# Kernel tuning notes

Measured on AMD Instinct MI355X. Metric: run time of the kernel, lower is better.

## Reference

```python
import jax, jax.numpy as jnp
import numpy as np

LN_EPS = 1e-5
NEG_SLOPE = 0.01  # torch F.leaky_relu default


def setup_inputs() -> dict:
    key = jax.random.key(0)
    ks = jax.random.split(key, 12)
    B, N, Do, Na = 128, 32, 128, 16
    H, Dk, Dv = 4, 64, 64
    Dio = Do + Na  # 144
    g = lambda k, shape, fan_in: jax.random.normal(k, shape, jnp.float32) / np.sqrt(fan_in)
    return {
        "states": jax.random.normal(ks[0], (B, N, Do), jnp.float32),
        "policies": jax.random.uniform(ks[1], (B, N, Na), jnp.float32),
        "actions": jax.random.uniform(ks[2], (B, N, Na), jnp.float32),
        "W_se": g(ks[3], (Do, 128), Do),
        "b_se": jnp.zeros((128,), jnp.float32),
        "W_sape": g(ks[4], (Dio, 128), Dio),
        "b_sape": jnp.zeros((128,), jnp.float32),
        "Wk": g(ks[5], (H, 128, Dk), 128),
        "Wq": g(ks[6], (H, 128, Dk), 128),
        "Wv": g(ks[7], (H, 128, Dv), 128),
        "ln_g": jnp.ones((H, Dv), jnp.float32),
        "ln_b": jnp.zeros((H, Dv), jnp.float32),
        "W_f1": g(ks[8], (H * Dv, 64), H * Dv),
        "W_f2": g(ks[9], (64, 1), 64),
    }


def _layernorm(x, g, b):
    mu = x.mean(-1, keepdims=True)
    var = ((x - mu) ** 2).mean(-1, keepdims=True)
    return (x - mu) * jax.lax.rsqrt(var + LN_EPS) * g + b


def reference(states, policies, actions, W_se, b_se, W_sape, b_sape,
              Wk, Wq, Wv, ln_g, ln_b, W_f1, W_f2):
    leaky = lambda x: jax.nn.leaky_relu(x, NEG_SLOPE)
    B, N, _ = states.shape
    H, _, Dv = Wv.shape
    d_k = Wk.shape[-1]

    se = leaky(states @ W_se + b_se)  # [B,N,128]

    oa = jnp.concatenate([states, actions], axis=-1)   # [B,N,Dio]
    op = jnp.concatenate([states, policies], axis=-1)  # [B,N,Dio]
    # oap[b,j,k] = op[b,k] if j==k else oa[b,k]  (place_policies/place_actions masks)
    eye = jnp.eye(N, dtype=states.dtype)[None, :, :, None]  # [1,N,N,1]
    oap = eye * op[:, None, :, :] + (1.0 - eye) * oa[:, None, :, :]  # [B,N,N,Dio]
    x = leaky(oap @ W_sape + b_sape)  # [B,N,N,128]

    key = jnp.einsum('bnd,hde->bhne', se, Wk)  # [B,H,N,Dk]
    qry = jnp.einsum('bnd,hde->bhne', se, Wq)
    scores = jnp.einsum('bhie,bhke->bhik', qry, key) / jnp.sqrt(jnp.asarray(d_k, states.dtype))
    w = jax.nn.softmax(scores, axis=-1)  # [B,H,N,N]

    av = jnp.einsum('bjkd,hde->bhjke', x, Wv)  # [B,H,N,N,Dv]
    # node_features[b,h,i,j] = sum_k w[b,h,i,k] * av[b,h,j,k]  (fuses torch's O(N^3) repeat)
    nf = jnp.einsum('bhik,bhjke->bhije', w, av)  # [B,H,N,N,Dv]
    nf = _layernorm(nf, ln_g[None, :, None, None, :], ln_b[None, :, None, None, :])

    mh = jnp.moveaxis(nf, 1, 3).reshape(B, N, N, H * Dv)  # concat heads on last dim
    value = leaky(mh @ W_f1) @ W_f2  # [B,N,N,1]
    return value, w
```

## Files before the change

### kernel.cpp

```cpp
#include <hip/hip_runtime.h>
#include <hip/hip_bf16.h>

#define B 128
#define N 32
#define DO 128
#define NA 16
#define H 4
#define DK 64
#define DV 64
#define LN_EPS 1e-5f
#define NEG_SLOPE 0.01f

typedef unsigned short u16;
typedef __attribute__((ext_vector_type(8))) short bf16x8;
typedef __attribute__((ext_vector_type(4))) float f32x4;

__device__ __forceinline__ float leaky(float x) {
    return x >= 0.f ? x : NEG_SLOPE * x;
}

__device__ __forceinline__ u16 f2bf(float x) {
    union { float f; unsigned int u; } v; v.f = x;
    unsigned int r = (v.u + 0x7FFF + ((v.u >> 16) & 1)) >> 16;
    return (u16)r;
}

__device__ __forceinline__ float bf2f(u16 x) {
    union { unsigned int u; float f; } v; v.u = ((unsigned int)x) << 16;
    return v.f;
}

__global__ __launch_bounds__(256) void kP(
    const float* __restrict__ Wk, const float* __restrict__ Wq,
    const float* __restrict__ Wv, const float* __restrict__ W_se,
    const float* __restrict__ W_sape, const float* __restrict__ ln_g,
    const float* __restrict__ ln_b, const float* __restrict__ W_f1,
    u16* __restrict__ wTb, u16* __restrict__ wseT, u16* __restrict__ wsapeT,
    u16* __restrict__ sapeTail, u16* __restrict__ wTg,
    float* __restrict__ GW, float* __restrict__ BW)
{
    const int blk = blockIdx.x;
    const int t   = threadIdx.x;
    __shared__ float wls[8192];

    if (blk < 4) {
        const int hh = blk;
        for (int m = 0; m < 3; m++) {
            const float* src = (m == 0 ? Wq : (m == 1 ? Wk : Wv)) + hh * 8192;
            for (int idx = t; idx < 2048; idx += 256)
                ((float4*)wls)[idx] = ((const float4*)src)[idx];
            __syncthreads();
            u16* dst = wTb + (hh * 3 + m) * 8192;
            for (int idx = t; idx < 8192; idx += 256) {
                const int n = idx >> 7, k = idx & 127;
                dst[idx] = f2bf(wls[k * 64 + n]);
            }
            __syncthreads();
        }
    } else if (blk == 4 || blk == 5) {
        const float* src = (blk == 4) ? W_se : W_sape;
        u16* dst = (blk == 4) ? wseT : wsapeT;
        for (int chunk = 0; chunk < 2; chunk++) {
            const int k0 = chunk * 64;
            for (int idx = t; idx < 2048; idx += 256)
                ((float4*)wls)[idx] = ((const float4*)(src + k0 * 128))[idx];
            __syncthreads();
            for (int idx = t; idx < 8192; idx += 256) {
                const int n = idx >> 6, kk = idx & 63;
                dst[n * 128 + k0 + kk] = f2bf(wls[kk * 128 + n]);
            }
            __syncthreads();
        }
        if (blk == 5) {
            for (int idx = t; idx < 2048; idx += 256)
                wls[idx] = W_sape[128 * 128 + idx];
            __syncthreads();
            for (int idx = t; idx < 4096; idx += 256) {
                const int n = idx >> 5, kk = idx & 31;
                sapeTail[n * 32 + kk] = (kk < 16) ? f2bf(wls[kk * 128 + n]) : (u16)0;
            }
        }
    } else {
        for (int idx = t; idx < 16384; idx += 256) {
            const int hh = idx >> 12, c = (idx >> 6) & 63, ee = idx & 63;
            wTg[idx] = f2bf(ln_g[hh * 64 + ee] * W_f1[(hh * 64 + ee) * 64 + c]);
        }
        {
            const int hh = t >> 6, c = t & 63;
            float g = 0.f;
            #pragma unroll 4
            for (int ee = 0; ee < 64; ee++)
                g += ln_g[hh * 64 + ee] * W_f1[(hh * 64 + ee) * 64 + c];
            GW[t] = g;
        }
        {
            const int c = t & 63, qq = t >> 6;
            float bacc = 0.f;
            #pragma unroll 4
            for (int r = 0; r < 64; r++)
                bacc += ln_b[qq * 64 + r] * W_f1[(qq * 64 + r) * 64 + c];
            wls[qq * 64 + c] = bacc;
        }
        __syncthreads();
        if (t < 64) BW[t] = wls[t] + wls[64 + t] + wls[128 + t] + wls[192 + t];
    }
}

__global__ __launch_bounds__(1024, 8) void kB(
    const float* __restrict__ states, const float* __restrict__ actions,
    const float* __restrict__ policies,
    const float* __restrict__ b_se, const float* __restrict__ b_sape,
    const u16* __restrict__ wTb, const u16* __restrict__ wseT,
    const u16* __restrict__ wsapeT, const u16* __restrict__ sapeTail,
    const u16* __restrict__ wTg,
    float* __restrict__ w_out,
    float* __restrict__ SG, float* __restrict__ DG,
    float* __restrict__ sumS, float* __restrict__ sumS2,
    float* __restrict__ sumD, float* __restrict__ sumD2,
    float* __restrict__ dotSD)
{
    const int bh   = blockIdx.x;
    const int b    = bh >> 2;
    const int h    = bh & 3;
    const int t    = threadIdx.x;
    const int wave = t >> 6;
    const int e    = t & 63;
    const int q16  = e >> 4;
    const int l16  = e & 15;

    __shared__ alignas(16) u16   sST[32 * 136];
    __shared__ alignas(16) u16   actA[32 * 40];
    __shared__ alignas(16) u16   polA[32 * 40];
    __shared__ alignas(16) u16   sSE[32 * 136];
    __shared__ alignas(16) u16   sXA[32 * 136];
    __shared__ alignas(16) u16   sXP[32 * 136];
    __shared__ alignas(16) u16   qb[32 * 72];
    __shared__ alignas(16) u16   kb[32 * 72];
    __shared__ alignas(16) u16   avaT[64 * 40];
    __shared__ alignas(16) u16   diffb[32 * 72];
    __shared__ alignas(16) u16   wb[32 * 40];
    __shared__ alignas(16) float S32[32 * 68];
    __shared__ alignas(16) u16   Sb[32 * 72];

    {
        const int r = t >> 5, c4 = (t & 31) * 4;
        const float4 s4 = *(const float4*)&states[(b * 32 + r) * 128 + c4];
        ushort4 u;
        u.x = f2bf(s4.x); u.y = f2bf(s4.y); u.z = f2bf(s4.z); u.w = f2bf(s4.w);
        *(ushort4*)&sST[r * 136 + c4] = u;
    }
    if (t < 512) {
        const int r = t >> 4, c = t & 15;
        actA[r * 40 + c]      = f2bf(actions[(b * 32 + r) * 16 + c]);
        actA[r * 40 + 16 + c] = 0;
    } else {
        const int t2 = t - 512, r = t2 >> 4, c = t2 & 15;
        polA[r * 40 + c]      = f2bf(policies[(b * 32 + r) * 16 + c]);
        polA[r * 40 + 16 + c] = 0;
    }
    __syncthreads();

    {
        const int mt = wave >> 3, nt = wave & 7;
        const int arow = mt * 16 + l16;
        const int bcol = nt * 16 + l16;
        f32x4 a_se = {0.f,0.f,0.f,0.f}, a_sp = {0.f,0.f,0.f,0.f};
        f32x4 a_oa = {0.f,0.f,0.f,0.f}, a_op = {0.f,0.f,0.f,0.f};
        const u16* bse_p = wseT + bcol * 128;
        const u16* bsp_p = wsapeT + bcol * 128;
        #pragma unroll
        for (int ks = 0; ks < 4; ks++) {
            const bf16x8 af = *(const bf16x8*)&sST[arow * 136 + ks * 32 + q16 * 8];
            a_se = __builtin_amdgcn_mfma_f32_16x16x32_bf16(
                af, *(const bf16x8*)&bse_p[ks * 32 + q16 * 8], a_se, 0, 0, 0);
            a_sp = __builtin_amdgcn_mfma_f32_16x16x32_bf16(
                af, *(const bf16x8*)&bsp_p[ks * 32 + q16 * 8], a_sp, 0, 0, 0);
        }
        const bf16x8 bt = *(const bf16x8*)&sapeTail[bcol * 32 + q16 * 8];
        a_oa = __builtin_amdgcn_mfma_f32_16x16x32_bf16(
            *(const bf16x8*)&actA[arow * 40 + q16 * 8], bt, a_oa, 0, 0, 0);
        a_op = __builtin_amdgcn_mfma_f32_16x16x32_bf16(
            *(const bf16x8*)&polA[arow * 40 + q16 * 8], bt, a_op, 0, 0, 0);
        const float bse_c = b_se[bcol];
        const float bsp_c = b_sape[bcol];
        const int r0 = mt * 16 + q16 * 4;
        #pragma unroll
        for (int v = 0; v < 4; v++) {
            sSE[(r0 + v) * 136 + bcol] = f2bf(leaky(a_se[v] + bse_c));
            sXA[(r0 + v) * 136 + bcol] = f2bf(leaky(a_sp[v] + a_oa[v] + bsp_c));
            sXP[(r0 + v) * 136 + bcol] = f2bf(leaky(a_sp[v] + a_op[v] + bsp_c));
        }
    }
    __syncthreads();

    f32x4 acc[2];
    #pragma unroll
    for (int p = 0; p < 2; p++) {
        const int tau = wave * 2 + p;
        const int mat = tau >> 3;
        const int mt  = (tau >> 2) & 1, nt = tau & 3;
        const u16* X  = (mat <= 1) ? sSE : (mat == 2 ? sXA : sXP);
        const int widx = (mat == 0) ? 0 : (mat == 1 ? 1 : 2);
        const int arow = mt * 16 + l16;
        const u16* wsrc = wTb + ((h * 3 + widx) * 64 + nt * 16 + l16) * 128;
        f32x4 a = {0.f, 0.f, 0.f, 0.f};
        #pragma unroll
        for (int ks = 0; ks < 4; ks++) {
            const bf16x8 af = *(const bf16x8*)&X[arow * 136 + ks * 32 + q16 * 8];
            const bf16x8 bf = *(const bf16x8*)&wsrc[ks * 32 + q16 * 8];
            a = __builtin_amdgcn_mfma_f32_16x16x32_bf16(af, bf, a, 0, 0, 0);
        }
        acc[p] = a;
    }
    #pragma unroll
    for (int p = 0; p < 2; p++) {
        const int tau = wave * 2 + p;
        const int mat = tau >> 3;
        const int mt  = (tau >> 2) & 1, nt = tau & 3;
        const int c   = nt * 16 + l16;
        const int r0  = mt * 16 + q16 * 4;
        if (mat == 0) {
            #pragma unroll
            for (int v = 0; v < 4; v++) qb[(r0 + v) * 72 + c] = f2bf(acc[p][v]);
        } else if (mat == 1) {
            #pragma unroll
            for (int v = 0; v < 4; v++) kb[(r0 + v) * 72 + c] = f2bf(acc[p][v]);
        } else if (mat == 2) {
            #pragma unroll
            for (int v = 0; v < 4; v++) avaT[c * 40 + (r0 + v)] = f2bf(acc[p][v]);
        }
    }
    __syncthreads();

    if (wave < 2) {
        const int mt = wave;
        f32x4 s0 = {0.f,0.f,0.f,0.f}, s1 = {0.f,0.f,0.f,0.f};
        #pragma unroll
        for (int ks = 0; ks < 2; ks++) {
            const bf16x8 af = *(const bf16x8*)&qb[(mt * 16 + l16) * 72 + ks * 32 + q16 * 8];
            const bf16x8 b0 = *(const bf16x8*)&kb[l16 * 72 + ks * 32 + q16 * 8];
            const bf16x8 b1 = *(const bf16x8*)&kb[(16 + l16) * 72 + ks * 32 + q16 * 8];
            s0 = __builtin_amdgcn_mfma_f32_16x16x32_bf16(af, b0, s0, 0, 0, 0);
            s1 = __builtin_amdgcn_mfma_f32_16x16x32_bf16(af, b1, s1, 0, 0, 0);
        }
        #pragma unroll
        for (int v = 0; v < 4; v++) {
            float a0 = s0[v] * 0.125f, a1 = s1[v] * 0.125f;
            float mx = fmaxf(a0, a1);
            #pragma unroll
            for (int m = 1; m < 16; m <<= 1) mx = fmaxf(mx, __shfl_xor(mx, m));
            float e0 = __expf(a0 - mx), e1 = __expf(a1 - mx);
            float sm = e0 + e1;
            #pragma unroll
            for (int m = 1; m < 16; m <<= 1) sm += __shfl_xor(sm, m);
            const float inv = 1.f / sm;
            e0 *= inv; e1 *= inv;
            const int i = mt * 16 + q16 * 4 + v;
            wb[i * 40 + l16]      = f2bf(e0);
            wb[i * 40 + 16 + l16] = f2bf(e1);
            w_out[(bh * 32 + i) * 32 + l16]      = e0;
            w_out[(bh * 32 + i) * 32 + 16 + l16] = e1;
        }
    } else if (wave >= 12) {
        #pragma unroll
        for (int p = 0; p < 2; p++) {
            const int tau = wave * 2 + p;
            const int mt  = (tau >> 2) & 1, nt = tau & 3;
            const int c   = nt * 16 + l16;
            const int r0  = mt * 16 + q16 * 4;
            #pragma unroll
            for (int v = 0; v < 4; v++) {
                const float av = bf2f(avaT[c * 40 + (r0 + v)]);
                diffb[(r0 + v) * 72 + c] = f2bf(acc[p][v] - av);
            }
        }
    }
    __syncthreads();

    if (wave < 8) {
        const int mt = wave >> 2, nt = wave & 3;
        const bf16x8 af = *(const bf16x8*)&wb[(mt * 16 + l16) * 40 + q16 * 8];
        const bf16x8 bf = *(const bf16x8*)&avaT[(nt * 16 + l16) * 40 + q16 * 8];
        f32x4 a = {0.f, 0.f, 0.f, 0.f};
        a = __builtin_amdgcn_mfma_f32_16x16x32_bf16(af, bf, a, 0, 0, 0);
        const int c = nt * 16 + l16, r0 = mt * 16 + q16 * 4;
        #pragma unroll
        for (int v = 0; v < 4; v++) {
            S32[(r0 + v) * 68 + c] = a[v];
            Sb[(r0 + v) * 72 + c]  = f2bf(a[v]);
        }
    } else {
        const int w8 = wave - 8;
        const int mt = w8 >> 2, nt = w8 & 3;
        const u16* wgp = wTg + (h * 64 + nt * 16 + l16) * 64;
        f32x4 a = {0.f, 0.f, 0.f, 0.f};
        #pragma unroll
        for (int ks = 0; ks < 2; ks++) {
            const bf16x8 af = *(const bf16x8*)&diffb[(mt * 16 + l16) * 72 + ks * 32 + q16 * 8];
            const bf16x8 bf = *(const bf16x8*)&wgp[ks * 32 + q16 * 8];
            a = __builtin_amdgcn_mfma_f32_16x16x32_bf16(af, bf, a, 0, 0, 0);
        }
        const int c = nt * 16 + l16, r0 = mt * 16 + q16 * 4;
        #pragma unroll
        for (int v = 0; v < 4; v++)
            DG[(bh * 32 + r0 + v) * 64 + c] = a[v];
    }
    if (t < 32) {
        float s1 = 0.f, s2 = 0.f;
        #pragma unroll
        for (int e8 = 0; e8 < 8; e8++) {
            const uint4 u = *(const uint4*)&diffb[t * 72 + e8 * 8];
            const unsigned int uu[4] = {u.x, u.y, u.z, u.w};
            #pragma unroll
            for (int q = 0; q < 4; q++) {
                const float fl = __uint_as_float(uu[q] << 16);
                const float fh = __uint_as_float(uu[q] & 0xffff0000u);
                s1 += fl + fh;
                s2 += fl * fl + fh * fh;
            }
        }
        sumD[bh * 32 + t] = s1; sumD2[bh * 32 + t] = s2;
    }
    __syncthreads();

    if (wave < 4) {
        const int mt = wave >> 1, nt = wave & 1;
        f32x4 a = {0.f, 0.f, 0.f, 0.f};
        #pragma unroll
        for (int ks = 0; ks < 2; ks++) {
            const bf16x8 af = *(const bf16x8*)&Sb[(mt * 16 + l16) * 72 + ks * 32 + q16 * 8];
            const bf16x8 bf = *(const bf16x8*)&diffb[(nt * 16 + l16) * 72 + ks * 32 + q16 * 8];
            a = __builtin_amdgcn_mfma_f32_16x16x32_bf16(af, bf, a, 0, 0, 0);
        }
        const int j = nt * 16 + l16, r0 = mt * 16 + q16 * 4;
        #pragma unroll
        for (int v = 0; v < 4; v++)
            dotSD[(bh * 32 + r0 + v) * 32 + j] = a[v];
    } else if (wave >= 8) {
        const int w8 = wave - 8;
        const int mt = w8 >> 2, nt = w8 & 3;
        const u16* wgp = wTg + (h * 64 + nt * 16 + l16) * 64;
        f32x4 a = {0.f, 0.f, 0.f, 0.f};
        #pragma unroll
        for (int ks = 0; ks < 2; ks++) {
            const bf16x8 af = *(const bf16x8*)&Sb[(mt * 16 + l16) * 72 + ks * 32 + q16 * 8];
            const bf16x8 bf = *(const bf16x8*)&wgp[ks * 32 + q16 * 8];
            a = __builtin_amdgcn_mfma_f32_16x16x32_bf16(af, bf, a, 0, 0, 0);
        }
        const int c = nt * 16 + l16, r0 = mt * 16 + q16 * 4;
        #pragma unroll
        for (int v = 0; v < 4; v++)
            SG[(bh * 32 + r0 + v) * 64 + c] = a[v];
    } else if (t >= 256 && t < 288) {
        const int r = t - 256;
        float s1 = 0.f, s2 = 0.f;
        #pragma unroll
        for (int e4 = 0; e4 < 16; e4++) {
            const float4 v4 = *(const float4*)&S32[r * 68 + e4 * 4];
            s1 += v4.x + v4.y + v4.z + v4.w;
            s2 += v4.x * v4.x + v4.y * v4.y + v4.z * v4.z + v4.w * v4.w;
        }
        sumS[bh * 32 + r] = s1; sumS2[bh * 32 + r] = s2;
    }
}

__global__ __launch_bounds__(256) void kC(
    const float* __restrict__ SG, const float* __restrict__ DG,
    const float* __restrict__ sumS, const float* __restrict__ sumS2,
    const float* __restrict__ sumD, const float* __restrict__ sumD2,
    const float* __restrict__ dotSD, const float* __restrict__ w_all,
    const float* __restrict__ GW, const float* __restrict__ BW,
    const float* __restrict__ W_f2, float* __restrict__ value)
{
    const int blk = blockIdx.x;
    const int b   = blk >> 2;
    const int i0  = (blk & 3) * 8;
    const int t   = threadIdx.x;

    __shared__ float SGs[8][256];
    __shared__ float GWs[256];
    __shared__ float BWs[64], wf2s[64];
    __shared__ float w_s[4][8][32];
    __shared__ float mu_s[4][8][32];
    __shared__ float inv_s[4][8][32];

    GWs[t] = GW[t];
    if (t < 64) { BWs[t] = BW[t]; wf2s[t] = W_f2[t]; }
    for (int idx4 = t; idx4 < 512; idx4 += 256) {
        const int ii  = idx4 >> 6;
        const int hc4 = idx4 & 63;
        const int hh  = hc4 >> 4, c4 = (hc4 & 15) * 4;
        ((float4*)&SGs[ii][0])[hc4] =
            *(const float4*)&SG[((b * 4 + hh) * 32 + i0 + ii) * 64 + c4];
    }
    for (int idx = t; idx < 1024; idx += 256) {
        const int hh = idx >> 8, ii = (idx >> 5) & 7, j = idx & 31;
        const int hi = (b * 4 + hh) * 32 + (i0 + ii);
        const int hj = (b * 4 + hh) * 32 + j;
        const float wv  = w_all[hi * 32 + j];
        const float dsd = dotSD[hi * 32 + j];
        const float mu  = (sumS[hi] + wv * sumD[hj]) * (1.f / 64.f);
        const float e2  = (sumS2[hi] + 2.f * wv * dsd + wv * wv * sumD2[hj]) * (1.f / 64.f);
        const float var = fmaxf(e2 - mu * mu, 0.f);
        w_s[hh][ii][j]   = wv;
        mu_s[hh][ii][j]  = mu;
        inv_s[hh][ii][j] = rsqrtf(var + LN_EPS);
    }
    __syncthreads();

    const int w0 = t >> 6;
    const int e  = t & 63;
    const float GW0 = GWs[e],       GW1 = GWs[64 + e];
    const float GW2 = GWs[128 + e], GW3 = GWs[192 + e];
    const float bwr = BWs[e], f2 = wf2s[e];
    const float* DGb = DG + b * H * N * 64;

    for (int jb = 0; jb < 8; jb++) {
        const int j = jb * 4 + w0;
        const float d0 = DGb[(0 * 32 + j) * 64 + e];
        const float d1 = DGb[(1 * 32 + j) * 64 + e];
        const float d2 = DGb[(2 * 32 + j) * 64 + e];
        const float d3 = DGb[(3 * 32 + j) * 64 + e];
        #pragma unroll
        for (int ii = 0; ii < 8; ii++) {
            float z = bwr;
            z += inv_s[0][ii][j] * (SGs[ii][e]       + w_s[0][ii][j] * d0 - mu_s[0][ii][j] * GW0);
            z += inv_s[1][ii][j] * (SGs[ii][64 + e]  + w_s[1][ii][j] * d1 - mu_s[1][ii][j] * GW1);
            z += inv_s[2][ii][j] * (SGs[ii][128 + e] + w_s[2][ii][j] * d2 - mu_s[2][ii][j] * GW2);
            z += inv_s[3][ii][j] * (SGs[ii][192 + e] + w_s[3][ii][j] * d3 - mu_s[3][ii][j] * GW3);
            float p = leaky(z) * f2;
            #pragma unroll
            for (int m = 32; m; m >>= 1) p += __shfl_xor(p, m);
            if (e == 0) value[(b * 32 + i0 + ii) * 32 + j] = p;
        }
    }
}

extern "C" void kernel_launch(void* const* d_in, const int* in_sizes, int n_in,
                              void* d_out, int out_size, void* d_ws, size_t ws_size,
                              hipStream_t stream)
{
    const float* states   = (const float*)d_in[0];
    const float* policies = (const float*)d_in[1];
    const float* actions  = (const float*)d_in[2];
    const float* W_se     = (const float*)d_in[3];
    const float* b_se     = (const float*)d_in[4];
    const float* W_sape   = (const float*)d_in[5];
    const float* b_sape   = (const float*)d_in[6];
    const float* Wk       = (const float*)d_in[7];
    const float* Wq       = (const float*)d_in[8];
    const float* Wv       = (const float*)d_in[9];
    const float* ln_g     = (const float*)d_in[10];
    const float* ln_b     = (const float*)d_in[11];
    const float* W_f1     = (const float*)d_in[12];
    const float* W_f2     = (const float*)d_in[13];

    float* out_value = (float*)d_out;
    float* out_w     = out_value + B * N * N;

    float* ws    = (float*)d_ws;
    float* SG    = ws;
    float* DG    = SG    + 1048576;
    float* sumS  = DG    + 1048576;
    float* sumS2 = sumS  + 16384;
    float* sumD  = sumS2 + 16384;
    float* sumD2 = sumD  + 16384;
    float* dotSD = sumD2 + 16384;
    float* GW    = dotSD + 524288;
    float* BW    = GW    + 256;
    u16*   wTb   = (u16*)(BW + 64);
    u16*   wseT  = wTb   + 98304;
    u16*   wsapeT= wseT  + 16384;
    u16*   sapeTail = wsapeT + 16384;
    u16*   wTg   = sapeTail + 4096;

    kP<<<7, 256, 0, stream>>>(Wk, Wq, Wv, W_se, W_sape, ln_g, ln_b, W_f1,
                              wTb, wseT, wsapeT, sapeTail, wTg, GW, BW);
    kB<<<B * H, 1024, 0, stream>>>(states, actions, policies, b_se, b_sape,
                                   wTb, wseT, wsapeT, sapeTail, wTg, out_w,
                                   SG, DG, sumS, sumS2, sumD, sumD2, dotSD);
    kC<<<512, 256, 0, stream>>>(SG, DG, sumS, sumS2, sumD, sumD2, dotSD,
                                out_w, GW, BW, W_f2, out_value);
}
```

Measured before the change: 149.1 us.

## Restructure final value kernel: split j across blocks, packed LN records, DPP reduction

The final kC kernel now launches twice as many blocks, each handling 16 j columns instead of 32. Per-(i,j,h) LayerNorm coefficients are pre-multiplied (inv, inv*w, -inv*mu) and packed so each inner step reads three vector LDS loads. SG and GW values are kept in registers instead of shared memory. The 64-lane cross-lane sum now uses DPP row operations instead of shuffle-xor. This trims LDS traffic and reduction latency in the epilogue, which is a small part of total time next to the main kernel kB.

```diff
diff --git a/kernel.cpp b/kernel.cpp
--- a/kernel.cpp
+++ b/kernel.cpp
@@ -28,6 +28,12 @@
 __device__ __forceinline__ float bf2f(u16 x) {
     union { unsigned int u; float f; } v; v.u = ((unsigned int)x) << 16;
     return v.f;
+}
+
+template<int CTRL>
+__device__ __forceinline__ float dppadd(float x) {
+    return x + __int_as_float(__builtin_amdgcn_update_dpp(
+        0, __float_as_int(x), CTRL, 0xF, 0xF, true));
 }
 
 __global__ __launch_bounds__(256) void kP(
@@ -373,65 +379,70 @@
     const float* __restrict__ W_f2, float* __restrict__ value)
 {
     const int blk = blockIdx.x;
-    const int b   = blk >> 2;
-    const int i0  = (blk & 3) * 8;
+    const int b   = blk >> 3;
+    const int i0  = ((blk >> 1) & 3) * 8;
+    const int j0  = (blk & 1) * 16;
     const int t   = threadIdx.x;
-
-    __shared__ float SGs[8][256];
-    __shared__ float GWs[256];
-    __shared__ float BWs[64], wf2s[64];
-    __shared__ float w_s[4][8][32];
-    __shared__ float mu_s[4][8][32];
-    __shared__ float inv_s[4][8][32];
-
-    GWs[t] = GW[t];
-    if (t < 64) { BWs[t] = BW[t]; wf2s[t] = W_f2[t]; }
-    for (int idx4 = t; idx4 < 512; idx4 += 256) {
-        const int ii  = idx4 >> 6;
-        const int hc4 = idx4 & 63;
-        const int hh  = hc4 >> 4, c4 = (hc4 & 15) * 4;
-        ((float4*)&SGs[ii][0])[hc4] =
-            *(const float4*)&SG[((b * 4 + hh) * 32 + i0 + ii) * 64 + c4];
-    }
-    for (int idx = t; idx < 1024; idx += 256) {
-        const int hh = idx >> 8, ii = (idx >> 5) & 7, j = idx & 31;
-        const int hi = (b * 4 + hh) * 32 + (i0 + ii);
+    const int w0  = t >> 6;
+    const int e   = t & 63;
+
+    __shared__ alignas(16) float pk[8 * 16 * 12];
+
+    for (int idx = t; idx < 512; idx += 256) {
+        const int ii = idx >> 6, jl = (idx >> 2) & 15, hh = idx & 3;
+        const int j  = j0 + jl;
+        const int hi = (b * 4 + hh) * 32 + i0 + ii;
         const int hj = (b * 4 + hh) * 32 + j;
         const float wv  = w_all[hi * 32 + j];
         const float dsd = dotSD[hi * 32 + j];
         const float mu  = (sumS[hi] + wv * sumD[hj]) * (1.f / 64.f);
         const float e2  = (sumS2[hi] + 2.f * wv * dsd + wv * wv * sumD2[hj]) * (1.f / 64.f);
         const float var = fmaxf(e2 - mu * mu, 0.f);
-        w_s[hh][ii][j]   = wv;
-        mu_s[hh][ii][j]  = mu;
-        inv_s[hh][ii][j] = rsqrtf(var + LN_EPS);
-    }
-    __syncthreads();
-
-    const int w0 = t >> 6;
-    const int e  = t & 63;
-    const float GW0 = GWs[e],       GW1 = GWs[64 + e];
-    const float GW2 = GWs[128 + e], GW3 = GWs[192 + e];
-    const float bwr = BWs[e], f2 = wf2s[e];
-    const float* DGb = DG + b * H * N * 64;
-
-    for (int jb = 0; jb < 8; jb++) {
-        const int j = jb * 4 + w0;
-        const float d0 = DGb[(0 * 32 + j) * 64 + e];
-        const float d1 = DGb[(1 * 32 + j) * 64 + e];
-        const float d2 = DGb[(2 * 32 + j) * 64 + e];
-        const float d3 = DGb[(3 * 32 + j) * 64 + e];
+        const float inv = rsqrtf(var + LN_EPS);
+        float* rec = &pk[(ii * 16 + jl) * 12 + hh * 3];
+        rec[0] = inv;
+        rec[1] = inv * wv;
+        rec[2] = -inv * mu;
+    }
+
+    const float bwr = BW[e];
+    const float f2v = W_f2[e];
+    float gw[4], sg[8][4];
+    #pragma unroll
+    for (int hh = 0; hh < 4; hh++) {
+        gw[hh] = GW[hh * 64 + e];
+        #pragma unroll
+        for (int ii = 0; ii < 8; ii++)
+            sg[ii][hh] = SG[((b * 4 + hh) * 32 + i0 + ii) * 64 + e];
+    }
+    __syncthreads();
+
+    for (int jb = 0; jb < 4; jb++) {
+        const int jl = jb * 4 + w0;
+        const int j  = j0 + jl;
+        float d[4];
+        #pragma unroll
+        for (int hh = 0; hh < 4; hh++)
+            d[hh] = DG[((b * 4 + hh) * 32 + j) * 64 + e];
         #pragma unroll
         for (int ii = 0; ii < 8; ii++) {
+            const float* rec = &pk[(ii * 16 + jl) * 12];
+            const f32x4 r0 = *(const f32x4*)rec;
+            const f32x4 r1 = *(const f32x4*)(rec + 4);
+            const f32x4 r2 = *(const f32x4*)(rec + 8);
             float z = bwr;
-            z += inv_s[0][ii][j] * (SGs[ii][e]       + w_s[0][ii][j] * d0 - mu_s[0][ii][j] * GW0);
-            z += inv_s[1][ii][j] * (SGs[ii][64 + e]  + w_s[1][ii][j] * d1 - mu_s[1][ii][j] * GW1);
-            z += inv_s[2][ii][j] * (SGs[ii][128 + e] + w_s[2][ii][j] * d2 - mu_s[2][ii][j] * GW2);
-            z += inv_s[3][ii][j] * (SGs[ii][192 + e] + w_s[3][ii][j] * d3 - mu_s[3][ii][j] * GW3);
-            float p = leaky(z) * f2;
-            #pragma unroll
-            for (int m = 32; m; m >>= 1) p += __shfl_xor(p, m);
-            if (e == 0) value[(b * 32 + i0 + ii) * 32 + j] = p;
+            z += r0[0] * sg[ii][0]; z += r0[1] * d[0]; z += r0[2] * gw[0];
+            z += r0[3] * sg[ii][1]; z += r1[0] * d[1]; z += r1[1] * gw[1];
+            z += r1[2] * sg[ii][2]; z += r1[3] * d[2]; z += r2[0] * gw[2];
+            z += r2[1] * sg[ii][3]; z += r2[2] * d[3]; z += r2[3] * gw[3];
+            float p = leaky(z) * f2v;
+            p = dppadd<0x111>(p);
+            p = dppadd<0x112>(p);
+            p = dppadd<0x114>(p);
+            p = dppadd<0x118>(p);
+            p = dppadd<0x142>(p);
+            p = dppadd<0x143>(p);
+            if (e == 63) value[(b * 32 + i0 + ii) * 32 + j] = p;
         }
     }
 }
@@ -479,6 +490,6 @@
     kB<<<B * H, 1024, 0, stream>>>(states, actions, policies, b_se, b_sape,
                                    wTb, wseT, wsapeT, sapeTail, wTg, out_w,
                                    SG, DG, sumS, sumS2, sumD, sumD2, dotSD);
-    kC<<<512, 256, 0, stream>>>(SG, DG, sumS, sumS2, sumD, sumD2, dotSD,
-                                out_w, GW, BW, W_f2, out_value);
-}
+    kC<<<B * 8, 256, 0, stream>>>(SG, DG, sumS, sumS2, sumD, sumD2, dotSD,
+                                  out_w, GW, BW, W_f2, out_value);
+}
```

Result: faster. 133.9 us (-10.2%).
